# Performance work log

Hardware: AMD Instinct MI355X
Metric: run time of the kernel (lower is better)

Reference implementation:

```python
import jax, jax.numpy as jnp
import numpy as np

B, S, H, R, IN, OPS, NPAD = 128, 128, 512, 16, 2, 5, 16
L = IN + NPAD
NEG = -1e12


def setup_inputs():
    key = jax.random.key(0)
    ks = jax.random.split(key, 32)
    def n(k, shape, scale=1.0):
        return jax.random.normal(k, shape, jnp.float32) * scale
    s = 0.05
    return {
        "encoder_outputs": n(ks[0], (S, B, H)),
        "current_emb": n(ks[1], (B, 1, H)),
        "left_childs": n(ks[2], (B, H)),
        "padding_hidden": jnp.zeros((1, H), jnp.float32),
        "num_pades": n(ks[3], (B, NPAD, H)),
        "rule_scores": n(ks[4], (R, H)),
        "embedding_weight": n(ks[5], (1, IN, H)),
        "W_concat_l": n(ks[6], (H, H), s), "b_concat_l": jnp.zeros((H,)),
        "W_concat_lg": n(ks[7], (H, H), s), "b_concat_lg": jnp.zeros((H,)),
        "W_concat_r": n(ks[8], (2 * H, H), s), "b_concat_r": jnp.zeros((H,)),
        "W_concat_rg": n(ks[9], (2 * H, H), s), "b_concat_rg": jnp.zeros((H,)),
        "W_tree_attn": n(ks[10], (2 * H, H), s), "b_tree_attn": jnp.zeros((H,)),
        "W_tree_score": n(ks[11], (H, 1), s), "b_tree_score": jnp.zeros((1,)),
        "W_rule_attn": n(ks[12], (2 * H, H), s), "b_rule_attn": jnp.zeros((H,)),
        "W_rule_score": n(ks[13], (H, 1), s), "b_rule_score": jnp.zeros((1,)),
        "W_rp1": n(ks[14], (H, H), s), "b_rp1": jnp.zeros((H,)),
        "W_rp2": n(ks[15], (H, 1), s), "b_rp2": jnp.zeros((1,)),
        "W_sc_attn": n(ks[16], (3 * H, H), s), "b_sc_attn": jnp.zeros((H,)),
        "W_sc_score": n(ks[17], (H, 1), s),
        "W_ops": n(ks[18], (2 * H, OPS), s), "b_ops": jnp.zeros((OPS,)),
        "seq_mask": jax.random.randint(ks[19], (B, S), 0, 2).astype(jnp.int32),
        "mask_nums": jax.random.randint(ks[20], (B, L), 0, 2).astype(jnp.int32),
        "has_left": jax.random.randint(ks[21], (B,), 0, 2).astype(jnp.int32),
        "stack_empty": jax.random.randint(ks[22], (B,), 0, 2).astype(jnp.int32),
    }


def reference(encoder_outputs, current_emb, left_childs, padding_hidden, num_pades,
              rule_scores, embedding_weight,
              W_concat_l, b_concat_l, W_concat_lg, b_concat_lg,
              W_concat_r, b_concat_r, W_concat_rg, b_concat_rg,
              W_tree_attn, b_tree_attn, W_tree_score, b_tree_score,
              W_rule_attn, b_rule_attn, W_rule_score, b_rule_score,
              W_rp1, b_rp1, W_rp2, b_rp2,
              W_sc_attn, b_sc_attn, W_sc_score, W_ops, b_ops,
              seq_mask, mask_nums, has_left, stack_empty):
    sm = seq_mask.astype(bool)          # [B,S] True = pad
    nm = mask_nums.astype(bool)         # [B,L]
    hl = has_left.astype(bool)[:, None]
    se = stack_empty.astype(bool)[:, None]
    h = encoder_outputs.shape[-1]
    # gather top-of-stack embedding, padding for empty stacks (the ragged python loop)
    c = jnp.where(se, padding_hidden[0], current_emb[:, 0])  # [B,H]
    # gated combine: left_child==None branch vs cat(left, c) branch (dropout=eval)
    node_l = jnp.tanh(c @ W_concat_l + b_concat_l) * jax.nn.sigmoid(c @ W_concat_lg + b_concat_lg)
    node_r = (jnp.tanh(left_childs @ W_concat_r[:h] + c @ W_concat_r[h:] + b_concat_r)
              * jax.nn.sigmoid(left_childs @ W_concat_rg[:h] + c @ W_concat_rg[h:] + b_concat_rg))
    q = jnp.where(hl, node_r, node_l)                        # [B,H]
    current_node = q[:, None, :]                              # [B,1,H]
    # TreeAttn: concat(hidden, enc) -> Linear -> tanh -> Linear(H,1) -> softmax over S
    e = jnp.tanh(q @ W_tree_attn[:h] + encoder_outputs @ W_tree_attn[h:] + b_tree_attn)  # [S,B,H]
    ae = (e @ W_tree_score)[..., 0] + b_tree_score[0]         # [S,B]
    ae = jnp.where(sm, NEG, ae.T)                             # [B,S]
    current_attn = jax.nn.softmax(ae, axis=1)                 # [B,S]
    current_context = jnp.einsum('bs,sbh->bh', current_attn, encoder_outputs)[:, None, :]
    # RuleAttn: concat(enc, rule) additive attention, softmax over S
    re = jnp.tanh(encoder_outputs @ W_rule_attn[:h]
                  + (rule_scores @ W_rule_attn[h:])[:, None, None, :]
                  + b_rule_attn)                              # [R,S,B,H]
    r_ae = (re @ W_rule_score)[..., 0] + b_rule_score[0]      # [R,S,B]
    r_ae = jnp.transpose(r_ae, (2, 0, 1))                     # [B,R,S]
    r_ae = jnp.where(sm[:, None, :], NEG, r_ae)
    rules_attn = jax.nn.softmax(r_ae, axis=-1)
    rules_context = jnp.einsum('brs,sbh->brh', rules_attn + 0.2 * current_attn[:, None, :], encoder_outputs)
    rule_prob = jax.nn.softmax((jnp.tanh(rules_context @ W_rp1 + b_rp1) @ W_rp2)[..., 0] + b_rp2[0], axis=-1)  # [B,R]
    # leaf scoring: Score(cat(node, context), [const_embs | num_pades])
    bsz = q.shape[0]
    ew = jnp.concatenate([jnp.broadcast_to(embedding_weight, (bsz,) + embedding_weight.shape[1:]), num_pades], axis=1)  # [B,L,H]
    leaf = jnp.concatenate([q, current_context[:, 0]], axis=1)  # [B,2H]
    sc = jnp.tanh((leaf @ W_sc_attn[:2 * h])[:, None, :] + ew @ W_sc_attn[2 * h:] + b_sc_attn)  # [B,L,H]
    num_score = jnp.where(nm, NEG, (sc @ W_sc_score)[..., 0])   # [B,L]
    op = leaf @ W_ops + b_ops                                   # [B,OPS]
    return num_score, op, current_node, current_context, ew, rule_prob
```

## Files before the change

### kernel.cpp

```cpp
#include <hip/hip_runtime.h>
#include <hip/hip_bf16.h>

#define B_ 128
#define S_ 128
#define H_ 512
#define R_ 16
#define IN_ 2
#define OPS_ 5
#define NPAD_ 16
#define L_ 18
#define NEGV (-1000000000000.0f)
#define C2_ (-2.885390081777927f)

typedef __bf16 bf16_t;
typedef bf16_t bf16x8 __attribute__((ext_vector_type(8)));
typedef float floatx4 __attribute__((ext_vector_type(4)));

__device__ __forceinline__ float rcp_f(float x) { return __builtin_amdgcn_rcpf(x); }
__device__ __forceinline__ float exp2_f(float x) { return __builtin_amdgcn_exp2f(x); }

__device__ __forceinline__ float fast_tanh(float x) {
    return 2.0f * rcp_f(1.0f + exp2_f(C2_ * x)) - 1.0f;
}
__device__ __forceinline__ float fast_sigmoid(float x) {
    return rcp_f(1.0f + exp2_f(-1.4426950408889634f * x));
}
__device__ __forceinline__ unsigned short f2bf(float f) {
    unsigned int u = __builtin_bit_cast(unsigned int, f);
    u += 0x7fff + ((u >> 16) & 1);
    return (unsigned short)(u >> 16);
}
__device__ __forceinline__ float bf2f(unsigned short u) {
    return __builtin_bit_cast(float, (unsigned int)u << 16);
}

#define LSTR 40
#define LBUF (128 * LSTR)

__device__ __forceinline__ void mfma_tile(const unsigned short* __restrict__ A,
                                          const unsigned short* __restrict__ Bt,
                                          void* __restrict__ Cv, bool bf16_out,
                                          int m0, int n0, int K, int ldc,
                                          unsigned short* As, unsigned short* Bs) {
    const int tid  = threadIdx.x;
    const int wid  = tid >> 6, lane = tid & 63;
    const int quad = lane >> 4, mn = lane & 15;
    const int wm = (wid & 1) * 64, wn = (wid >> 1) * 64;
    const int sr = tid >> 2;
    const int sc = (tid & 3) * 8;

    const unsigned short* pa0 = A  + (size_t)(m0 + sr)      * K + sc;
    const unsigned short* pa1 = A  + (size_t)(m0 + sr + 64) * K + sc;
    const unsigned short* pb0 = Bt + (size_t)(n0 + sr)      * K + sc;
    const unsigned short* pb1 = Bt + (size_t)(n0 + sr + 64) * K + sc;

    uint4 a0 = *(const uint4*)pa0;
    uint4 a1 = *(const uint4*)pa1;
    uint4 b0 = *(const uint4*)pb0;
    uint4 b1 = *(const uint4*)pb1;
    *(uint4*)&As[sr * LSTR + sc]        = a0;
    *(uint4*)&As[(sr + 64) * LSTR + sc] = a1;
    *(uint4*)&Bs[sr * LSTR + sc]        = b0;
    *(uint4*)&Bs[(sr + 64) * LSTR + sc] = b1;
    if (K > 32) {
        a0 = *(const uint4*)(pa0 + 32);
        a1 = *(const uint4*)(pa1 + 32);
        b0 = *(const uint4*)(pb0 + 32);
        b1 = *(const uint4*)(pb1 + 32);
    }
    __syncthreads();

    floatx4 acc[4][4] = {};

    for (int k0 = 0; k0 < K; k0 += 32) {
        const int cur = (k0 >> 5) & 1;
        unsigned short* Asb = As + cur * LBUF;
        unsigned short* Bsb = Bs + cur * LBUF;

        bf16x8 af[4], bfr[4];
        #pragma unroll
        for (int i = 0; i < 4; ++i)
            af[i] = *(const bf16x8*)&Asb[(wm + i * 16 + mn) * LSTR + quad * 8];
        #pragma unroll
        for (int j = 0; j < 4; ++j)
            bfr[j] = *(const bf16x8*)&Bsb[(wn + j * 16 + mn) * LSTR + quad * 8];

        #pragma unroll
        for (int i = 0; i < 4; ++i)
            #pragma unroll
            for (int j = 0; j < 4; ++j)
                acc[i][j] = __builtin_amdgcn_mfma_f32_16x16x32_bf16(bfr[j], af[i], acc[i][j], 0, 0, 0);

        if (k0 + 32 < K) {
            unsigned short* Asn = As + (cur ^ 1) * LBUF;
            unsigned short* Bsn = Bs + (cur ^ 1) * LBUF;
            *(uint4*)&Asn[sr * LSTR + sc]        = a0;
            *(uint4*)&Asn[(sr + 64) * LSTR + sc] = a1;
            *(uint4*)&Bsn[sr * LSTR + sc]        = b0;
            *(uint4*)&Bsn[(sr + 64) * LSTR + sc] = b1;
            if (k0 + 64 < K) {
                a0 = *(const uint4*)(pa0 + k0 + 64);
                a1 = *(const uint4*)(pa1 + k0 + 64);
                b0 = *(const uint4*)(pb0 + k0 + 64);
                b1 = *(const uint4*)(pb1 + k0 + 64);
            }
            __syncthreads();
        }
    }

    #pragma unroll
    for (int i = 0; i < 4; ++i) {
        int row = m0 + wm + i * 16 + mn;
        #pragma unroll
        for (int j = 0; j < 4; ++j) {
            int col = n0 + wn + j * 16 + quad * 4;
            if (bf16_out) {
                ushort4 v = {f2bf(acc[i][j][0]), f2bf(acc[i][j][1]),
                             f2bf(acc[i][j][2]), f2bf(acc[i][j][3])};
                *(ushort4*)((unsigned short*)Cv + (size_t)row * ldc + col) = v;
            } else {
                float4 v = {acc[i][j][0], acc[i][j][1], acc[i][j][2], acc[i][j][3]};
                *(float4*)((float*)Cv + (size_t)row * ldc + col) = v;
            }
        }
    }
}

__global__ __launch_bounds__(256) void k_gemm_mega1(const unsigned short* __restrict__ EO_bf,
                                                    const unsigned short* __restrict__ Wcat,
                                                    unsigned short* __restrict__ eobuf,
                                                    const unsigned short* __restrict__ q_bf,
                                                    const unsigned short* __restrict__ T5,
                                                    float* __restrict__ qT) {
    __shared__ unsigned short As[2 * LBUF];
    __shared__ unsigned short Bs[2 * LBUF];
    int blk = blockIdx.x;
    if (blk < 1024)
        mfma_tile(EO_bf, Wcat, eobuf, true, (blk & 127) * 128, (blk >> 7) * 128, 512, 1024, As, Bs);
    else
        mfma_tile(q_bf, T5, qT, false, 0, (blk - 1024) * 128, 512, 512, As, Bs);
}

__global__ __launch_bounds__(256) void k_gemm_mega2(const unsigned short* __restrict__ rctx_bf,
                                                    const unsigned short* __restrict__ T8,
                                                    float* __restrict__ rclin,
                                                    const unsigned short* __restrict__ leaf_bf,
                                                    const unsigned short* __restrict__ T9,
                                                    float* __restrict__ lsb,
                                                    const unsigned short* __restrict__ ew_bf,
                                                    const unsigned short* __restrict__ T10,
                                                    unsigned short* __restrict__ ewp_bf) {
    __shared__ unsigned short As[2 * LBUF];
    __shared__ unsigned short Bs[2 * LBUF];
    int blk = blockIdx.x;
    if (blk < 64)
        mfma_tile(rctx_bf, T8, rclin, false, (blk >> 2) * 128, (blk & 3) * 128, 512, 512, As, Bs);
    else if (blk < 68)
        mfma_tile(leaf_bf, T9, lsb, false, 0, (blk - 64) * 128, 1024, 512, As, Bs);
    else {
        int r = blk - 68;
        mfma_tile(ew_bf, T10, ewp_bf, true, (r >> 2) * 128, (r & 3) * 128, 512, 512, As, Bs);
    }
}

struct MJ5 {
    const unsigned short* A[5]; const unsigned short* Bt[5]; float* C[5];
    int M[5]; int K[5];
};
__global__ __launch_bounds__(256) void gemm_bf16_j5(MJ5 g) {
    __shared__ unsigned short As[2 * LBUF];
    __shared__ unsigned short Bs[2 * LBUF];

    const int z = blockIdx.z;
    const unsigned short* A  = g.A[z];
    const unsigned short* Bt = g.Bt[z];
    float* C = g.C[z];
    const int M = g.M[z], K = g.K[z];

    const int tid  = threadIdx.x;
    const int wid  = tid >> 6, lane = tid & 63;
    const int quad = lane >> 4, mn = lane & 15;
    const int wm = (wid & 1) * 64, wn = (wid >> 1) * 64;
    const int n0 = blockIdx.x * 128;

    const int sr = tid >> 2;
    const int sc = (tid & 3) * 8;
    const int ra0 = min(sr, M - 1);
    const int ra1 = min(sr + 64, M - 1);

    const unsigned short* pa0 = A  + (size_t)ra0 * K + sc;
    const unsigned short* pa1 = A  + (size_t)ra1 * K + sc;
    const unsigned short* pb0 = Bt + (size_t)(n0 + sr)      * K + sc;
    const unsigned short* pb1 = Bt + (size_t)(n0 + sr + 64) * K + sc;

    uint4 a0 = *(const uint4*)pa0;
    uint4 a1 = *(const uint4*)pa1;
    uint4 b0 = *(const uint4*)pb0;
    uint4 b1 = *(const uint4*)pb1;
    *(uint4*)&As[sr * LSTR + sc]        = a0;
    *(uint4*)&As[(sr + 64) * LSTR + sc] = a1;
    *(uint4*)&Bs[sr * LSTR + sc]        = b0;
    *(uint4*)&Bs[(sr + 64) * LSTR + sc] = b1;
    if (K > 32) {
        a0 = *(const uint4*)(pa0 + 32);
        a1 = *(const uint4*)(pa1 + 32);
        b0 = *(const uint4*)(pb0 + 32);
        b1 = *(const uint4*)(pb1 + 32);
    }
    __syncthreads();

    floatx4 acc[4][4] = {};

    for (int k0 = 0; k0 < K; k0 += 32) {
        const int cur = (k0 >> 5) & 1;
        unsigned short* Asb = As + cur * LBUF;
        unsigned short* Bsb = Bs + cur * LBUF;

        bf16x8 af[4], bfr[4];
        #pragma unroll
        for (int i = 0; i < 4; ++i)
            af[i] = *(const bf16x8*)&Asb[(wm + i * 16 + mn) * LSTR + quad * 8];
        #pragma unroll
        for (int j = 0; j < 4; ++j)
            bfr[j] = *(const bf16x8*)&Bsb[(wn + j * 16 + mn) * LSTR + quad * 8];

        #pragma unroll
        for (int i = 0; i < 4; ++i)
            #pragma unroll
            for (int j = 0; j < 4; ++j)
                acc[i][j] = __builtin_amdgcn_mfma_f32_16x16x32_bf16(bfr[j], af[i], acc[i][j], 0, 0, 0);

        if (k0 + 32 < K) {
            unsigned short* Asn = As + (cur ^ 1) * LBUF;
            unsigned short* Bsn = Bs + (cur ^ 1) * LBUF;
            *(uint4*)&Asn[sr * LSTR + sc]        = a0;
            *(uint4*)&Asn[(sr + 64) * LSTR + sc] = a1;
            *(uint4*)&Bsn[sr * LSTR + sc]        = b0;
            *(uint4*)&Bsn[(sr + 64) * LSTR + sc] = b1;
            if (k0 + 64 < K) {
                a0 = *(const uint4*)(pa0 + k0 + 64);
                a1 = *(const uint4*)(pa1 + k0 + 64);
                b0 = *(const uint4*)(pb0 + k0 + 64);
                b1 = *(const uint4*)(pb1 + k0 + 64);
            }
            __syncthreads();
        }
    }

    #pragma unroll
    for (int i = 0; i < 4; ++i) {
        int row = wm + i * 16 + mn;
        if (row < M) {
            #pragma unroll
            for (int j = 0; j < 4; ++j) {
                int col = n0 + wn + j * 16 + quad * 4;
                float4 v = {acc[i][j][0], acc[i][j][1], acc[i][j][2], acc[i][j][3]};
                *(float4*)(C + (size_t)row * 512 + col) = v;
            }
        }
    }
}

struct PrepArgs {
    const float *EO, *cur, *padh, *left, *rsc, *embw, *npad;
    const int* se;
    unsigned short *EO_bf, *c_bf, *acat_bf, *rsc_bf, *ew_bf;
    float* ew_out;
    const float* tsrc[11];
    unsigned short* tdst[11];
    int tK[11];
    int tbase[12];
};
#define PG_CAST 8192
#define PG_EW   1152
#define PG_PREP 288
#define PG_WT   3584
#define PG_TOTAL (PG_CAST + PG_EW + PG_PREP + PG_WT)

__global__ __launch_bounds__(256) void k_prep_mega(PrepArgs a) {
    __shared__ float t[32][33];
    int blk = blockIdx.x, tid = threadIdx.x;
    if (blk < PG_CAST) {
        int i = (blk * 256 + tid) * 4;
        float4 v = *(const float4*)(a.EO + i);
        ushort4 o;
        o.x = f2bf(v.x); o.y = f2bf(v.y); o.z = f2bf(v.z); o.w = f2bf(v.w);
        *(ushort4*)(a.EO_bf + i) = o;
    } else if (blk < PG_CAST + PG_EW) {
        int i = ((blk - PG_CAST) * 256 + tid) * 4;
        int j = i & 511;
        int bl = i >> 9;
        int l = bl % L_;
        int b = bl / L_;
        const float* src = (l < IN_) ? (a.embw + l * H_ + j)
                                     : (a.npad + ((size_t)b * NPAD_ + (l - IN_)) * H_ + j);
        float4 v = *(const float4*)src;
        *(float4*)(a.ew_out + i) = v;
        ushort4 o;
        o.x = f2bf(v.x); o.y = f2bf(v.y); o.z = f2bf(v.z); o.w = f2bf(v.w);
        *(ushort4*)(a.ew_bf + i) = o;
    } else if (blk < PG_CAST + PG_EW + PG_PREP) {
        int i = (blk - PG_CAST - PG_EW) * 256 + tid;
        if (i < B_ * H_) {
            int b = i >> 9, j = i & 511;
            float cv = a.se[b] ? a.padh[j] : a.cur[i];
            a.c_bf[i] = f2bf(cv);
            a.acat_bf[b * 1024 + j] = f2bf(a.left[i]);
            a.acat_bf[b * 1024 + 512 + j] = f2bf(cv);
        } else {
            int k = i - B_ * H_;
            a.rsc_bf[k] = f2bf(a.rsc[k]);
        }
    } else {
        int rel = blk - (PG_CAST + PG_EW + PG_PREP);
        int j = 0;
        while (rel >= a.tbase[j + 1]) ++j;
        int r = rel - a.tbase[j];
        int K = a.tK[j];
        const float* src = a.tsrc[j];
        unsigned short* dst = a.tdst[j];
        int bx = (r & 15) * 32;
        int by = (r >> 4) * 32;
        int tx = tid & 31, ty = tid >> 5;
        #pragma unroll
        for (int i = 0; i < 32; i += 8)
            t[ty + i][tx] = src[(size_t)(by + ty + i) * 512 + bx + tx];
        __syncthreads();
        #pragma unroll
        for (int i = 0; i < 32; i += 8)
            dst[(size_t)(bx + ty + i) * K + by + tx] = f2bf(t[tx][ty + i]);
    }
}

__global__ void k_node(const float* __restrict__ gl, const float* __restrict__ glg,
                       const float* __restrict__ gr, const float* __restrict__ grg,
                       const float* __restrict__ bl, const float* __restrict__ blg,
                       const float* __restrict__ br, const float* __restrict__ brg,
                       const int* __restrict__ hl,
                       unsigned short* __restrict__ q_bf, float* __restrict__ node_out,
                       unsigned short* __restrict__ leaf_bf) {
    int i = blockIdx.x * blockDim.x + threadIdx.x;
    int b = i >> 9, j = i & 511;
    float nl = fast_tanh(gl[i] + bl[j]) * fast_sigmoid(glg[i] + blg[j]);
    float nr = fast_tanh(gr[i] + br[j]) * fast_sigmoid(grg[i] + brg[j]);
    float v = hl[b] ? nr : nl;
    node_out[i] = v;
    q_bf[i] = f2bf(v);
    leaf_bf[b * 1024 + j] = f2bf(v);
}

__global__ __launch_bounds__(256) void k_score_fused(const float* __restrict__ qT,
                                                     const unsigned short* __restrict__ eobuf,
                                                     const float* __restrict__ b_ta,
                                                     const float* __restrict__ w_ts,
                                                     const float* __restrict__ b_ts,
                                                     const float* __restrict__ RP,
                                                     const float* __restrict__ b_ra,
                                                     const float* __restrict__ w_rs,
                                                     const float* __restrict__ b_rs,
                                                     const int* __restrict__ sm,
                                                     float* __restrict__ attn,
                                                     float* __restrict__ comb) {
    __shared__ float sc[S_];
    int blk = blockIdx.x;
    int tid = threadIdx.x;
    int wid = tid >> 6, lane = tid & 63;
    int j0 = lane * 8;

    if (blk < 128) {
        int b = blk;
        float4 q0 = *(const float4*)(qT + b * H_ + j0);
        float4 q1 = *(const float4*)(qT + b * H_ + j0 + 4);
        float4 t0 = *(const float4*)(b_ta + j0);
        float4 t1 = *(const float4*)(b_ta + j0 + 4);
        float4 w0 = *(const float4*)(w_ts + j0);
        float4 w1 = *(const float4*)(w_ts + j0 + 4);
        float qc[8] = {C2_*(q0.x+t0.x), C2_*(q0.y+t0.y), C2_*(q0.z+t0.z), C2_*(q0.w+t0.w),
                       C2_*(q1.x+t1.x), C2_*(q1.y+t1.y), C2_*(q1.z+t1.z), C2_*(q1.w+t1.w)};
        float w2[8] = {2*w0.x, 2*w0.y, 2*w0.z, 2*w0.w, 2*w1.x, 2*w1.y, 2*w1.z, 2*w1.w};
        float wsum = 0.5f * (w2[0]+w2[1]+w2[2]+w2[3]+w2[4]+w2[5]+w2[6]+w2[7]);
        float bias = b_ts[0];

        for (int s = wid; s < S_; s += 4) {
            if (sm[b * S_ + s]) {
                if (lane == 0) sc[s] = NEGV;
                continue;
            }
            uint4 ev = *(const uint4*)(eobuf + ((size_t)s * B_ + b) * 1024 + j0);
            const unsigned short* ep = (const unsigned short*)&ev;
            float acc = -wsum;
            #pragma unroll
            for (int k = 0; k < 8; ++k) {
                float y = fmaf(C2_, bf2f(ep[k]), qc[k]);
                acc = fmaf(w2[k], rcp_f(1.0f + exp2_f(y)), acc);
            }
            #pragma unroll
            for (int o = 32; o > 0; o >>= 1) acc += __shfl_xor(acc, o);
            if (lane == 0) sc[s] = acc + bias;
        }
        __syncthreads();
        if (tid < 64) {
            float v0 = sc[tid], v1 = sc[tid + 64];
            float m = fmaxf(v0, v1);
            #pragma unroll
            for (int o = 32; o > 0; o >>= 1) m = fmaxf(m, __shfl_xor(m, o));
            float e0 = __expf(v0 - m), e1 = __expf(v1 - m);
            float ss = e0 + e1;
            #pragma unroll
            for (int o = 32; o > 0; o >>= 1) ss += __shfl_xor(ss, o);
            float r = rcp_f(ss);
            attn[b * S_ + tid] = e0 * r;
            attn[b * S_ + tid + 64] = e1 * r;
        }
        return;
    }

    int row = (blk - 128) * 4 + wid;
    int s = row >> 7, b = row & 127;
    bool masked = sm[b * S_ + s] != 0;
    if (masked) {
        if (lane < R_) comb[((size_t)b * R_ + lane) * S_ + s] = NEGV;
        return;
    }
    uint4 ev = *(const uint4*)(eobuf + (size_t)row * 1024 + 512 + j0);
    const unsigned short* ep = (const unsigned short*)&ev;
    float4 a0 = *(const float4*)(b_ra + j0);
    float4 a1 = *(const float4*)(b_ra + j0 + 4);
    float4 w0 = *(const float4*)(w_rs + j0);
    float4 w1 = *(const float4*)(w_rs + j0 + 4);
    float ba[8] = {a0.x, a0.y, a0.z, a0.w, a1.x, a1.y, a1.z, a1.w};
    float w2[8], ed[8];
    float wsum = 0.f;
    {
        float w[8] = {w0.x, w0.y, w0.z, w0.w, w1.x, w1.y, w1.z, w1.w};
        #pragma unroll
        for (int k = 0; k < 8; ++k) {
            wsum += w[k];
            w2[k] = 2.0f * w[k];
            ed[k] = C2_ * (bf2f(ep[k]) + ba[k]);
        }
    }
    float bias = b_rs[0];
    #pragma unroll
    for (int r = 0; r < R_; ++r) {
        float4 r0 = *(const float4*)(RP + r * H_ + j0);
        float4 r1 = *(const float4*)(RP + r * H_ + j0 + 4);
        float rp[8] = {r0.x, r0.y, r0.z, r0.w, r1.x, r1.y, r1.z, r1.w};
        float acc = -wsum;
        #pragma unroll
        for (int k = 0; k < 8; ++k) {
            float y = fmaf(C2_, rp[k], ed[k]);
            acc = fmaf(w2[k], rcp_f(1.0f + exp2_f(y)), acc);
        }
        #pragma unroll
        for (int o = 32; o > 0; o >>= 1) acc += __shfl_xor(acc, o);
        if (lane == 0) comb[((size_t)b * R_ + r) * S_ + s] = acc + bias;
    }
}

__global__ __launch_bounds__(256) void k_ctxsm(const unsigned short* __restrict__ EO_bf,
                                               const float* __restrict__ attn,
                                               const float* __restrict__ comb,
                                               const int* __restrict__ sm,
                                               float* __restrict__ ctx_out,
                                               unsigned short* __restrict__ leaf_bf,
                                               unsigned short* __restrict__ rctx) {
    __shared__ float cb[R_ * S_];
    __shared__ float at[S_];
    __shared__ short usl[S_];
    __shared__ int ucount;
    int b = blockIdx.x;
    int tid = threadIdx.x;
    int w = tid >> 6, lane = tid & 63;

    if (tid < S_) at[tid] = attn[b * S_ + tid];
    for (int i = tid; i < R_ * S_; i += 256) cb[i] = comb[(size_t)b * R_ * S_ + i];
    if (tid == 0) {
        int c = 0;
        for (int s = 0; s < S_; ++s)
            if (!sm[b * S_ + s]) usl[c++] = (short)s;
        ucount = c;
    }
    __syncthreads();

    #pragma unroll
    for (int rr = 0; rr < 4; ++rr) {
        int r = w * 4 + rr;
        float v0 = cb[r * S_ + lane], v1 = cb[r * S_ + lane + 64];
        float m = fmaxf(v0, v1);
        #pragma unroll
        for (int o = 32; o > 0; o >>= 1) m = fmaxf(m, __shfl_xor(m, o));
        float e0 = __expf(v0 - m), e1 = __expf(v1 - m);
        float ss = e0 + e1;
        #pragma unroll
        for (int o = 32; o > 0; o >>= 1) ss += __shfl_xor(ss, o);
        float rc_ = rcp_f(ss);
        cb[r * S_ + lane]      = e0 * rc_ + 0.2f * at[lane];
        cb[r * S_ + lane + 64] = e1 * rc_ + 0.2f * at[lane + 64];
    }
    __syncthreads();

    int j = blockIdx.y * 256 + tid;
    int nu = ucount;
    float ctx = 0.f;
    float rc[R_] = {};
    #pragma unroll 2
    for (int ii = 0; ii < nu; ++ii) {
        int s = usl[ii];
        float eo = bf2f(EO_bf[((size_t)s * B_ + b) * H_ + j]);
        ctx += at[s] * eo;
        #pragma unroll
        for (int r = 0; r < R_; ++r) rc[r] += cb[r * S_ + s] * eo;
    }
    ctx_out[b * H_ + j] = ctx;
    leaf_bf[b * 1024 + 512 + j] = f2bf(ctx);
    #pragma unroll
    for (int r = 0; r < R_; ++r) rctx[((size_t)b * R_ + r) * H_ + j] = f2bf(rc[r]);
}

__global__ __launch_bounds__(256) void k_epilogue(const float* __restrict__ rclin,
                                                  const float* __restrict__ b_rp1,
                                                  const float* __restrict__ w_rp2,
                                                  const float* __restrict__ b_rp2,
                                                  float* __restrict__ prob,
                                                  const float* __restrict__ lsb,
                                                  const unsigned short* __restrict__ ewp,
                                                  const float* __restrict__ b_sc,
                                                  const float* __restrict__ w_scs,
                                                  const int* __restrict__ mask_nums,
                                                  float* __restrict__ ns_out,
                                                  const unsigned short* __restrict__ leaf_bf,
                                                  const float* __restrict__ Wops,
                                                  const float* __restrict__ bops,
                                                  float* __restrict__ op_out) {
    __shared__ float sc[R_];
    int blk = blockIdx.x;
    int wid = threadIdx.x >> 6, lane = threadIdx.x & 63;
    if (blk < 128) {
        int b = blk;
        int j0 = lane * 8;
        float4 p0 = *(const float4*)(b_rp1 + j0);
        float4 p1 = *(const float4*)(b_rp1 + j0 + 4);
        float4 w0 = *(const float4*)(w_rp2 + j0);
        float4 w1 = *(const float4*)(w_rp2 + j0 + 4);
        float brc[8] = {C2_*p0.x, C2_*p0.y, C2_*p0.z, C2_*p0.w,
                        C2_*p1.x, C2_*p1.y, C2_*p1.z, C2_*p1.w};
        float w[8] = {w0.x, w0.y, w0.z, w0.w, w1.x, w1.y, w1.z, w1.w};
        float wsum = 0.f;
        #pragma unroll
        for (int k = 0; k < 8; ++k) wsum += w[k];
        #pragma unroll
        for (int rr = 0; rr < 4; ++rr) {
            int r = wid * 4 + rr;
            const float* rl = rclin + ((size_t)b * R_ + r) * H_ + j0;
            float4 r0 = *(const float4*)(rl);
            float4 r1 = *(const float4*)(rl + 4);
            float rv[8] = {r0.x, r0.y, r0.z, r0.w, r1.x, r1.y, r1.z, r1.w};
            float acc = -wsum;
            #pragma unroll
            for (int k = 0; k < 8; ++k) {
                float y = fmaf(C2_, rv[k], brc[k]);
                acc = fmaf(2.0f * w[k], rcp_f(1.0f + exp2_f(y)), acc);
            }
            #pragma unroll
            for (int o = 32; o > 0; o >>= 1) acc += __shfl_xor(acc, o);
            if (lane == 0) sc[r] = acc + b_rp2[0];
        }
        __syncthreads();
        if (threadIdx.x < R_) {
            float m = -1e30f;
            for (int r = 0; r < R_; ++r) m = fmaxf(m, sc[r]);
            float sum = 0.f;
            for (int r = 0; r < R_; ++r) sum += __expf(sc[r] - m);
            prob[b * R_ + threadIdx.x] = __expf(sc[threadIdx.x] - m) * rcp_f(sum);
        }
    } else if (blk < 704) {
        int row = (blk - 128) * 4 + wid;
        int b = row / L_, l = row - b * L_;
        bool masked = mask_nums[b * L_ + l] != 0;
        if (masked) {
            if (lane == 0) ns_out[b * L_ + l] = NEGV;
            return;
        }
        int j0 = lane * 8;
        uint4 ev = *(const uint4*)(ewp + (size_t)row * H_ + j0);
        const unsigned short* ep = (const unsigned short*)&ev;
        float4 l0 = *(const float4*)(lsb + b * H_ + j0);
        float4 l1 = *(const float4*)(lsb + b * H_ + j0 + 4);
        float4 s0 = *(const float4*)(b_sc + j0);
        float4 s1 = *(const float4*)(b_sc + j0 + 4);
        float4 w0 = *(const float4*)(w_scs + j0);
        float4 w1 = *(const float4*)(w_scs + j0 + 4);
        float lc[8] = {C2_*(l0.x+s0.x), C2_*(l0.y+s0.y), C2_*(l0.z+s0.z), C2_*(l0.w+s0.w),
                       C2_*(l1.x+s1.x), C2_*(l1.y+s1.y), C2_*(l1.z+s1.z), C2_*(l1.w+s1.w)};
        float w[8] = {w0.x, w0.y, w0.z, w0.w, w1.x, w1.y, w1.z, w1.w};
        float wsum = 0.f;
        #pragma unroll
        for (int k = 0; k < 8; ++k) wsum += w[k];
        float acc = -wsum;
        #pragma unroll
        for (int k = 0; k < 8; ++k) {
            float y = fmaf(C2_, bf2f(ep[k]), lc[k]);
            acc = fmaf(2.0f * w[k], rcp_f(1.0f + exp2_f(y)), acc);
        }
        #pragma unroll
        for (int o = 32; o > 0; o >>= 1) acc += __shfl_xor(acc, o);
        if (lane == 0) ns_out[b * L_ + l] = acc;
    } else {
        int b = (blk - 704) * 4 + wid;
        int base = b * 1024 + lane * 16;
        uint4 v0 = *(const uint4*)(leaf_bf + base);
        uint4 v1 = *(const uint4*)(leaf_bf + base + 8);
        const unsigned short* lp0 = (const unsigned short*)&v0;
        const unsigned short* lp1 = (const unsigned short*)&v1;
        float lv[16];
        #pragma unroll
        for (int k = 0; k < 8; ++k) { lv[k] = bf2f(lp0[k]); lv[8 + k] = bf2f(lp1[k]); }
        #pragma unroll
        for (int o = 0; o < OPS_; ++o) {
            float acc = 0.f;
            #pragma unroll
            for (int k = 0; k < 16; ++k)
                acc = fmaf(lv[k], Wops[(size_t)(lane * 16 + k) * OPS_ + o], acc);
            #pragma unroll
            for (int of = 32; of > 0; of >>= 1) acc += __shfl_xor(acc, of);
            if (lane == 0) op_out[b * OPS_ + o] = acc + bops[o];
        }
    }
}

extern "C" void kernel_launch(void* const* d_in, const int* in_sizes, int n_in,
                              void* d_out, int out_size, void* d_ws, size_t ws_size,
                              hipStream_t stream) {
    const float* EO   = (const float*)d_in[0];
    const float* cur  = (const float*)d_in[1];
    const float* left = (const float*)d_in[2];
    const float* padh = (const float*)d_in[3];
    const float* npad = (const float*)d_in[4];
    const float* rsc  = (const float*)d_in[5];
    const float* embw = (const float*)d_in[6];
    const float* Wl   = (const float*)d_in[7];  const float* bl   = (const float*)d_in[8];
    const float* Wlg  = (const float*)d_in[9];  const float* blg  = (const float*)d_in[10];
    const float* Wr   = (const float*)d_in[11]; const float* br   = (const float*)d_in[12];
    const float* Wrg  = (const float*)d_in[13]; const float* brg  = (const float*)d_in[14];
    const float* Wta  = (const float*)d_in[15]; const float* bta  = (const float*)d_in[16];
    const float* Wts  = (const float*)d_in[17]; const float* bts  = (const float*)d_in[18];
    const float* Wra  = (const float*)d_in[19]; const float* bra  = (const float*)d_in[20];
    const float* Wrs  = (const float*)d_in[21]; const float* brs  = (const float*)d_in[22];
    const float* Wrp1 = (const float*)d_in[23]; const float* brp1 = (const float*)d_in[24];
    const float* Wrp2 = (const float*)d_in[25]; const float* brp2 = (const float*)d_in[26];
    const float* Wsa  = (const float*)d_in[27]; const float* bsa  = (const float*)d_in[28];
    const float* Wss  = (const float*)d_in[29];
    const float* Wops = (const float*)d_in[30]; const float* bops = (const float*)d_in[31];
    const int* smk = (const int*)d_in[32];
    const int* nmk = (const int*)d_in[33];
    const int* hlk = (const int*)d_in[34];
    const int* sek = (const int*)d_in[35];

    float* out = (float*)d_out;

    const size_t O_NS    = 0;
    const size_t O_OP    = O_NS + (size_t)B_ * L_;
    const size_t O_NODE  = O_OP + (size_t)B_ * OPS_;
    const size_t O_CTX   = O_NODE + (size_t)B_ * H_;
    const size_t O_EW    = O_CTX + (size_t)B_ * H_;
    const size_t O_RPROB = O_EW + (size_t)B_ * L_ * H_;

    float* f = (float*)d_ws;
    float* rp_buf = f;               f += 8192;
    float* qT     = f;               f += 65536;
    float* attn   = f;               f += 16384;
    float* comb   = f;               f += 262144;
    float* gl     = f;               f += 65536;
    float* glg    = f;               f += 65536;
    float* gr     = f;               f += 65536;
    float* grg    = f;               f += 65536;
    float* lsb    = f;               f += 65536;
    float* rclin  = f;               f += 1048576;
    unsigned short* u = (unsigned short*)f;
    unsigned short* EO_bf   = u;     u += 8388608;
    unsigned short* ew_bf   = u;     u += 1179648;
    unsigned short* leaf_bf = u;     u += 131072;
    unsigned short* rctx_bf = u;     u += 1048576;
    unsigned short* Wcat    = u;     u += 524288;
    unsigned short* T0      = u;     u += 262144;
    unsigned short* T1      = u;     u += 262144;
    unsigned short* T2      = u;     u += 524288;
    unsigned short* T3      = u;     u += 524288;
    unsigned short* T4      = u;     u += 262144;
    unsigned short* T5      = u;     u += 262144;
    unsigned short* T8      = u;     u += 262144;
    unsigned short* T9      = u;     u += 524288;
    unsigned short* T10     = u;     u += 262144;
    unsigned short* q_bf    = u;     u += 65536;
    unsigned short* c_bf    = u;     u += 65536;
    unsigned short* acat_bf = u;     u += 131072;
    unsigned short* rsc_bf  = u;     u += 8192;
    unsigned short* ewp_bf  = u;     u += 1179648;
    unsigned short* eobuf   = u;     u += 16777216;

    PrepArgs a;
    a.EO = EO; a.cur = cur; a.padh = padh; a.left = left; a.rsc = rsc;
    a.embw = embw; a.npad = npad; a.se = sek;
    a.EO_bf = EO_bf; a.c_bf = c_bf; a.acat_bf = acat_bf; a.rsc_bf = rsc_bf;
    a.ew_bf = ew_bf; a.ew_out = out + O_EW;
    const float* tsrc[11] = {Wl, Wlg, Wr, Wrg, Wra + (size_t)H_ * H_, Wta,
                             Wta + (size_t)H_ * H_, Wra, Wrp1, Wsa, Wsa + (size_t)2 * H_ * H_};
    unsigned short* tdst[11] = {T0, T1, T2, T3, T4, T5, Wcat, Wcat + 512 * 512, T8, T9, T10};
    int tk[11] = {512, 512, 1024, 1024, 512, 512, 512, 512, 512, 1024, 512};
    int base = 0;
    for (int i = 0; i < 11; ++i) {
        a.tsrc[i] = tsrc[i]; a.tdst[i] = tdst[i]; a.tK[i] = tk[i];
        a.tbase[i] = base;
        base += 16 * (tk[i] / 32);
    }
    a.tbase[11] = base;
    k_prep_mega<<<PG_TOTAL, 256, 0, stream>>>(a);

    MJ5 g;
    g.A[0] = c_bf;    g.Bt[0] = T0; g.C[0] = gl;     g.M[0] = B_;  g.K[0] = 512;
    g.A[1] = c_bf;    g.Bt[1] = T1; g.C[1] = glg;    g.M[1] = B_;  g.K[1] = 512;
    g.A[2] = acat_bf; g.Bt[2] = T2; g.C[2] = gr;     g.M[2] = B_;  g.K[2] = 1024;
    g.A[3] = acat_bf; g.Bt[3] = T3; g.C[3] = grg;    g.M[3] = B_;  g.K[3] = 1024;
    g.A[4] = rsc_bf;  g.Bt[4] = T4; g.C[4] = rp_buf; g.M[4] = R_;  g.K[4] = 512;
    gemm_bf16_j5<<<dim3(4, 1, 5), 256, 0, stream>>>(g);

    k_node<<<256, 256, 0, stream>>>(gl, glg, gr, grg, bl, blg, br, brg, hlk,
                                    q_bf, out + O_NODE, leaf_bf);

    k_gemm_mega1<<<1028, 256, 0, stream>>>(EO_bf, Wcat, eobuf, q_bf, T5, qT);

    k_score_fused<<<128 + S_ * B_ / 4, 256, 0, stream>>>(
        qT, eobuf, bta, Wts, bts, rp_buf, bra, Wrs, brs, smk, attn, comb);

    k_ctxsm<<<dim3(B_, 2), 256, 0, stream>>>(EO_bf, attn, comb, smk, out + O_CTX,
                                             leaf_bf, rctx_bf);

    k_gemm_mega2<<<140, 256, 0, stream>>>(rctx_bf, T8, rclin, leaf_bf, T9, lsb,
                                          ew_bf, T10, ewp_bf);

    k_epilogue<<<736, 256, 0, stream>>>(rclin, brp1, Wrp2, brp2, out + O_RPROB,
                                        lsb, ewp_bf, bsa, Wss, nmk, out + O_NS,
                                        leaf_bf, Wops, bops, out + O_OP);
}
```

Baseline: 284.7 us.

## Use direct global-to-LDS loads with XOR swizzle in GEMMs; transpose rule weights in ctx kernel

Both bf16 MFMA GEMM paths now stage tiles with global_load_lds (16-byte direct-to-LDS) into an unpadded, XOR-swizzled LDS layout. This replaces register-staged prefetch and padded rows, aiming to cut VGPR pressure and LDS store instructions while avoiding bank conflicts. The loads for the next tile are issued before the MFMAs, leaving one barrier per k-step. The context kernel also stores rule weights s-major with a stride of 20 so each step reads them as four float4 LDS loads, and the comb input is read straight from global memory. The swizzle and wave-base mapping must match the lane order that global_load_lds writes, so it carries a correctness risk.

Result: no change. 290.0 us (+1.9%).

```diff
diff --git a/kernel.cpp b/kernel.cpp
--- a/kernel.cpp
+++ b/kernel.cpp
@@ -34,8 +34,14 @@
     return __builtin_bit_cast(float, (unsigned int)u << 16);
 }
 
-#define LSTR 40
-#define LBUF (128 * LSTR)
+__device__ __forceinline__ void glds16(const void* g, void* l) {
+    __builtin_amdgcn_global_load_lds(
+        (const __attribute__((address_space(1))) void*)g,
+        (__attribute__((address_space(3))) void*)l, 16, 0, 0);
+}
+
+#define LROW 32
+#define LBUF 4096
 
 __device__ __forceinline__ void mfma_tile(const unsigned short* __restrict__ A,
                                           const unsigned short* __restrict__ Bt,
@@ -43,47 +49,47 @@
                                           int m0, int n0, int K, int ldc,
                                           unsigned short* As, unsigned short* Bs) {
     const int tid  = threadIdx.x;
-    const int wid  = tid >> 6, lane = tid & 63;
+    const int w    = tid >> 6, lane = tid & 63;
     const int quad = lane >> 4, mn = lane & 15;
-    const int wm = (wid & 1) * 64, wn = (wid >> 1) * 64;
+    const int wm = (w & 1) * 64, wn = (w >> 1) * 64;
     const int sr = tid >> 2;
-    const int sc = (tid & 3) * 8;
-
-    const unsigned short* pa0 = A  + (size_t)(m0 + sr)      * K + sc;
-    const unsigned short* pa1 = A  + (size_t)(m0 + sr + 64) * K + sc;
-    const unsigned short* pb0 = Bt + (size_t)(n0 + sr)      * K + sc;
-    const unsigned short* pb1 = Bt + (size_t)(n0 + sr + 64) * K + sc;
-
-    uint4 a0 = *(const uint4*)pa0;
-    uint4 a1 = *(const uint4*)pa1;
-    uint4 b0 = *(const uint4*)pb0;
-    uint4 b1 = *(const uint4*)pb1;
-    *(uint4*)&As[sr * LSTR + sc]        = a0;
-    *(uint4*)&As[(sr + 64) * LSTR + sc] = a1;
-    *(uint4*)&Bs[sr * LSTR + sc]        = b0;
-    *(uint4*)&Bs[(sr + 64) * LSTR + sc] = b1;
-    if (K > 32) {
-        a0 = *(const uint4*)(pa0 + 32);
-        a1 = *(const uint4*)(pa1 + 32);
-        b0 = *(const uint4*)(pb0 + 32);
-        b1 = *(const uint4*)(pb1 + 32);
-    }
+    const int csw = ((tid & 3) ^ ((tid >> 3) & 3)) * 8;
+    const int qs  = (quad ^ ((mn >> 1) & 3)) * 8;
+
+    const unsigned short* pa0 = A  + (size_t)(m0 + sr)      * K + csw;
+    const unsigned short* pa1 = A  + (size_t)(m0 + sr + 64) * K + csw;
+    const unsigned short* pb0 = Bt + (size_t)(n0 + sr)      * K + csw;
+    const unsigned short* pb1 = Bt + (size_t)(n0 + sr + 64) * K + csw;
+
+    const int wbase = w * 512;
+    glds16(pa0, As + wbase);
+    glds16(pa1, As + wbase + 2048);
+    glds16(pb0, Bs + wbase);
+    glds16(pb1, Bs + wbase + 2048);
     __syncthreads();
 
     floatx4 acc[4][4] = {};
 
     for (int k0 = 0; k0 < K; k0 += 32) {
         const int cur = (k0 >> 5) & 1;
-        unsigned short* Asb = As + cur * LBUF;
-        unsigned short* Bsb = Bs + cur * LBUF;
+        const unsigned short* Asb = As + cur * LBUF;
+        const unsigned short* Bsb = Bs + cur * LBUF;
+
+        if (k0 + 32 < K) {
+            const int nb = cur ^ 1;
+            glds16(pa0 + k0 + 32, As + nb * LBUF + wbase);
+            glds16(pa1 + k0 + 32, As + nb * LBUF + wbase + 2048);
+            glds16(pb0 + k0 + 32, Bs + nb * LBUF + wbase);
+            glds16(pb1 + k0 + 32, Bs + nb * LBUF + wbase + 2048);
+        }
 
         bf16x8 af[4], bfr[4];
         #pragma unroll
         for (int i = 0; i < 4; ++i)
-            af[i] = *(const bf16x8*)&Asb[(wm + i * 16 + mn) * LSTR + quad * 8];
+            af[i] = *(const bf16x8*)&Asb[(wm + i * 16 + mn) * LROW + qs];
         #pragma unroll
         for (int j = 0; j < 4; ++j)
-            bfr[j] = *(const bf16x8*)&Bsb[(wn + j * 16 + mn) * LSTR + quad * 8];
+            bfr[j] = *(const bf16x8*)&Bsb[(wn + j * 16 + mn) * LROW + qs];
 
         #pragma unroll
         for (int i = 0; i < 4; ++i)
@@ -91,21 +97,7 @@
             for (int j = 0; j < 4; ++j)
                 acc[i][j] = __builtin_amdgcn_mfma_f32_16x16x32_bf16(bfr[j], af[i], acc[i][j], 0, 0, 0);
 
-        if (k0 + 32 < K) {
-            unsigned short* Asn = As + (cur ^ 1) * LBUF;
-            unsigned short* Bsn = Bs + (cur ^ 1) * LBUF;
-            *(uint4*)&Asn[sr * LSTR + sc]        = a0;
-            *(uint4*)&Asn[(sr + 64) * LSTR + sc] = a1;
-            *(uint4*)&Bsn[sr * LSTR + sc]        = b0;
-            *(uint4*)&Bsn[(sr + 64) * LSTR + sc] = b1;
-            if (k0 + 64 < K) {
-                a0 = *(const uint4*)(pa0 + k0 + 64);
-                a1 = *(const uint4*)(pa1 + k0 + 64);
-                b0 = *(const uint4*)(pb0 + k0 + 64);
-                b1 = *(const uint4*)(pb1 + k0 + 64);
-            }
-            __syncthreads();
-        }
+        __syncthreads();
     }
 
     #pragma unroll
@@ -178,51 +170,51 @@
     const int M = g.M[z], K = g.K[z];
 
     const int tid  = threadIdx.x;
-    const int wid  = tid >> 6, lane = tid & 63;
+    const int w    = tid >> 6, lane = tid & 63;
     const int quad = lane >> 4, mn = lane & 15;
-    const int wm = (wid & 1) * 64, wn = (wid >> 1) * 64;
+    const int wm = (w & 1) * 64, wn = (w >> 1) * 64;
     const int n0 = blockIdx.x * 128;
 
     const int sr = tid >> 2;
-    const int sc = (tid & 3) * 8;
+    const int csw = ((tid & 3) ^ ((tid >> 3) & 3)) * 8;
+    const int qs  = (quad ^ ((mn >> 1) & 3)) * 8;
     const int ra0 = min(sr, M - 1);
     const int ra1 = min(sr + 64, M - 1);
 
-    const unsigned short* pa0 = A  + (size_t)ra0 * K + sc;
-    const unsigned short* pa1 = A  + (size_t)ra1 * K + sc;
-    const unsigned short* pb0 = Bt + (size_t)(n0 + sr)      * K + sc;
-    const unsigned short* pb1 = Bt + (size_t)(n0 + sr + 64) * K + sc;
-
-    uint4 a0 = *(const uint4*)pa0;
-    uint4 a1 = *(const uint4*)pa1;
-    uint4 b0 = *(const uint4*)pb0;
-    uint4 b1 = *(const uint4*)pb1;
-    *(uint4*)&As[sr * LSTR + sc]        = a0;
-    *(uint4*)&As[(sr + 64) * LSTR + sc] = a1;
-    *(uint4*)&Bs[sr * LSTR + sc]        = b0;
-    *(uint4*)&Bs[(sr + 64) * LSTR + sc] = b1;
-    if (K > 32) {
-        a0 = *(const uint4*)(pa0 + 32);
-        a1 = *(const uint4*)(pa1 + 32);
-        b0 = *(const uint4*)(pb0 + 32);
-        b1 = *(const uint4*)(pb1 + 32);
-    }
+    const unsigned short* pa0 = A  + (size_t)ra0 * K + csw;
+    const unsigned short* pa1 = A  + (size_t)ra1 * K + csw;
+    const unsigned short* pb0 = Bt + (size_t)(n0 + sr)      * K + csw;
+    const unsigned short* pb1 = Bt + (size_t)(n0 + sr + 64) * K + csw;
+
+    const int wbase = w * 512;
+    glds16(pa0, As + wbase);
+    glds16(pa1, As + wbase + 2048);
+    glds16(pb0, Bs + wbase);
+    glds16(pb1, Bs + wbase + 2048);
     __syncthreads();
 
     floatx4 acc[4][4] = {};
 
     for (int k0 = 0; k0 < K; k0 += 32) {
         const int cur = (k0 >> 5) & 1;
-        unsigned short* Asb = As + cur * LBUF;
-        unsigned short* Bsb = Bs + cur * LBUF;
+        const unsigned short* Asb = As + cur * LBUF;
+        const unsigned short* Bsb = Bs + cur * LBUF;
+
+        if (k0 + 32 < K) {
+            const int nb = cur ^ 1;
+            glds16(pa0 + k0 + 32, As + nb * LBUF + wbase);
+            glds16(pa1 + k0 + 32, As + nb * LBUF + wbase + 2048);
+            glds16(pb0 + k0 + 32, Bs + nb * LBUF + wbase);
+            glds16(pb1 + k0 + 32, Bs + nb * LBUF + wbase + 2048);
+        }
 
         bf16x8 af[4], bfr[4];
         #pragma unroll
         for (int i = 0; i < 4; ++i)
-            af[i] = *(const bf16x8*)&Asb[(wm + i * 16 + mn) * LSTR + quad * 8];
+            af[i] = *(const bf16x8*)&Asb[(wm + i * 16 + mn) * LROW + qs];
         #pragma unroll
         for (int j = 0; j < 4; ++j)
-            bfr[j] = *(const bf16x8*)&Bsb[(wn + j * 16 + mn) * LSTR + quad * 8];
+            bfr[j] = *(const bf16x8*)&Bsb[(wn + j * 16 + mn) * LROW + qs];
 
         #pragma unroll
         for (int i = 0; i < 4; ++i)
@@ -230,21 +222,7 @@
             for (int j = 0; j < 4; ++j)
                 acc[i][j] = __builtin_amdgcn_mfma_f32_16x16x32_bf16(bfr[j], af[i], acc[i][j], 0, 0, 0);
 
-        if (k0 + 32 < K) {
-            unsigned short* Asn = As + (cur ^ 1) * LBUF;
-            unsigned short* Bsn = Bs + (cur ^ 1) * LBUF;
-            *(uint4*)&Asn[sr * LSTR + sc]        = a0;
-            *(uint4*)&Asn[(sr + 64) * LSTR + sc] = a1;
-            *(uint4*)&Bsn[sr * LSTR + sc]        = b0;
-            *(uint4*)&Bsn[(sr + 64) * LSTR + sc] = b1;
-            if (k0 + 64 < K) {
-                a0 = *(const uint4*)(pa0 + k0 + 64);
-                a1 = *(const uint4*)(pa1 + k0 + 64);
-                b0 = *(const uint4*)(pb0 + k0 + 64);
-                b1 = *(const uint4*)(pb1 + k0 + 64);
-            }
-            __syncthreads();
-        }
+        __syncthreads();
     }
 
     #pragma unroll
@@ -465,7 +443,7 @@
                                                float* __restrict__ ctx_out,
                                                unsigned short* __restrict__ leaf_bf,
                                                unsigned short* __restrict__ rctx) {
-    __shared__ float cb[R_ * S_];
+    __shared__ float cb2[S_ * 20];
     __shared__ float at[S_];
     __shared__ short usl[S_];
     __shared__ int ucount;
@@ -474,7 +452,6 @@
     int w = tid >> 6, lane = tid & 63;
 
     if (tid < S_) at[tid] = attn[b * S_ + tid];
-    for (int i = tid; i < R_ * S_; i += 256) cb[i] = comb[(size_t)b * R_ * S_ + i];
     if (tid == 0) {
         int c = 0;
         for (int s = 0; s < S_; ++s)
@@ -486,7 +463,8 @@
     #pragma unroll
     for (int rr = 0; rr < 4; ++rr) {
         int r = w * 4 + rr;
-        float v0 = cb[r * S_ + lane], v1 = cb[r * S_ + lane + 64];
+        const float* rowp = comb + (size_t)b * R_ * S_ + r * S_;
+        float v0 = rowp[lane], v1 = rowp[lane + 64];
         float m = fmaxf(v0, v1);
         #pragma unroll
         for (int o = 32; o > 0; o >>= 1) m = fmaxf(m, __shfl_xor(m, o));
@@ -495,8 +473,8 @@
         #pragma unroll
         for (int o = 32; o > 0; o >>= 1) ss += __shfl_xor(ss, o);
         float rc_ = rcp_f(ss);
-        cb[r * S_ + lane]      = e0 * rc_ + 0.2f * at[lane];
-        cb[r * S_ + lane + 64] = e1 * rc_ + 0.2f * at[lane + 64];
+        cb2[lane * 20 + r]        = e0 * rc_ + 0.2f * at[lane];
+        cb2[(lane + 64) * 20 + r] = e1 * rc_ + 0.2f * at[lane + 64];
     }
     __syncthreads();
 
@@ -504,13 +482,22 @@
     int nu = ucount;
     float ctx = 0.f;
     float rc[R_] = {};
-    #pragma unroll 2
     for (int ii = 0; ii < nu; ++ii) {
         int s = usl[ii];
         float eo = bf2f(EO_bf[((size_t)s * B_ + b) * H_ + j]);
-        ctx += at[s] * eo;
-        #pragma unroll
-        for (int r = 0; r < R_; ++r) rc[r] += cb[r * S_ + s] * eo;
+        float4 c0 = *(const float4*)&cb2[s * 20];
+        float4 c1 = *(const float4*)&cb2[s * 20 + 4];
+        float4 c2 = *(const float4*)&cb2[s * 20 + 8];
+        float4 c3 = *(const float4*)&cb2[s * 20 + 12];
+        ctx = fmaf(at[s], eo, ctx);
+        rc[0]  = fmaf(c0.x, eo, rc[0]);  rc[1]  = fmaf(c0.y, eo, rc[1]);
+        rc[2]  = fmaf(c0.z, eo, rc[2]);  rc[3]  = fmaf(c0.w, eo, rc[3]);
+        rc[4]  = fmaf(c1.x, eo, rc[4]);  rc[5]  = fmaf(c1.y, eo, rc[5]);
+        rc[6]  = fmaf(c1.z, eo, rc[6]);  rc[7]  = fmaf(c1.w, eo, rc[7]);
+        rc[8]  = fmaf(c2.x, eo, rc[8]);  rc[9]  = fmaf(c2.y, eo, rc[9]);
+        rc[10] = fmaf(c2.z, eo, rc[10]); rc[11] = fmaf(c2.w, eo, rc[11]);
+        rc[12] = fmaf(c3.x, eo, rc[12]); rc[13] = fmaf(c3.y, eo, rc[13]);
+        rc[14] = fmaf(c3.z, eo, rc[14]); rc[15] = fmaf(c3.w, eo, rc[15]);
     }
     ctx_out[b * H_ + j] = ctx;
     leaf_bf[b * 1024 + 512 + j] = f2bf(ctx);
```
